# Performance work log

Hardware: AMD Instinct MI355X
Metric: run time of the kernel (lower is better)

Reference implementation:

```python
import jax, jax.numpy as jnp
import numpy as np

B = 100000      # query points
L = 8           # num levels
N_RBF = 256     # RBF centers per level
F = 16          # features per level
OUT = 3         # output dim


def setup_inputs() -> dict:
    key = jax.random.key(0)
    k = jax.random.split(key, 6)
    x = jax.random.normal(k[0], (B, 3), dtype=jnp.float32)
    # small-magnitude features so gaussian RBF responses are non-degenerate
    feats = 0.1 * jax.random.normal(k[1], (B, L * F), dtype=jnp.float32)
    # centers initialized uniform(-1e-4, 1e-4) as in the torch module
    centers = jax.random.uniform(k[2], (L, N_RBF, F), dtype=jnp.float32,
                                 minval=-1e-4, maxval=1e-4)
    # log-width parameters (exp'd in forward); small perturbation around 0
    betas = 0.01 * jax.random.normal(k[3], (L, N_RBF, F), dtype=jnp.float32)
    W = jax.random.normal(k[4], (OUT, N_RBF * L), dtype=jnp.float32) / np.sqrt(N_RBF * L)
    b = jax.random.normal(k[5], (OUT,), dtype=jnp.float32) * 0.01
    return {"x": x, "feats": feats, "centers": centers, "betas": betas, "W": W, "b": b}


def reference(x, feats, centers, betas, W, b):
    # centers, betas: [L, N, F]. x is unused by the original forward (faithful).
    Lnum, N, f = centers.shape
    rbfs = []
    for i in range(Lnum):
        # concat of first i+1 per-level tables along feature axis -> [N, (i+1)*f]
        C = centers[: i + 1].transpose(1, 0, 2).reshape(N, (i + 1) * f)
        Bw = jnp.exp(betas[: i + 1].transpose(1, 0, 2).reshape(N, (i + 1) * f))
        x_in = feats[:, : (i + 1) * f]                      # [B, (i+1)*f]
        term1 = (x_in * x_in) @ Bw.T                        # [B, N]
        term2 = x_in @ (Bw * C).T                           # [B, N]
        term3 = jnp.sum(Bw * C * C, axis=1)                 # [N]
        dist_sq = term1 - 2.0 * term2 + term3[None, :]
        rbfs.append(jnp.exp(-0.5 * dist_sq))                # gaussian basis
    outs = jnp.concatenate(rbfs, axis=-1)                   # [B, L*N]
    return outs @ W.T + b
```

## Files before the change

kernel.cpp:

```cpp
#include <hip/hip_runtime.h>
#include <math.h>

#define LN 8
#define NRBF 256
#define FD 16
#define OUTD 3

typedef __attribute__((ext_vector_type(8))) short short8;
typedef __attribute__((ext_vector_type(4))) float floatx4;

__device__ __forceinline__ short f2bf(float f) {
    unsigned u = __builtin_bit_cast(unsigned, f);
    u += 0x7fffu + ((u >> 16) & 1u);
    return (short)(u >> 16);
}


__global__ __launch_bounds__(256) void prep(
    const float* __restrict__ centers, const float* __restrict__ betas,
    const float* __restrict__ W, short* __restrict__ PKB, float* __restrict__ EPI)
{
    int t = blockIdx.x * 256 + threadIdx.x;
    if (t < 8192) {
        int lane = t & 63;
        int nt   = (t >> 6) & 15;
        int j    = t >> 10;
        int n    = nt * 16 + (lane & 15);
        int kq   = lane >> 4;
        short8 v;
#pragma unroll
        for (int e = 0; e < 8; ++e) {
            int k = kq * 8 + e;
            int m = k >> 1;
            int p = k & 1;
            size_t idx = ((size_t)(j * NRBF + n)) * FD + m;
            float a = __expf(betas[idx]);
            float c = centers[idx];
            v[e] = f2bf(p ? (-2.0f * a * c) : a);
        }
        *((short8*)(PKB + (size_t)t * 8)) = v;
    }
    if (t < 2048) {
        int j = t >> 8;
        int n = t & 255;
        float t3 = 0.f;
        for (int jj = 0; jj <= j; ++jj)
#pragma unroll
            for (int m = 0; m < FD; ++m) {
                size_t idx = ((size_t)(jj * NRBF + n)) * FD + m;
                float a = __expf(betas[idx]);
                float c = centers[idx];
                t3 = fmaf(a * c, c, t3);
            }
        int nt = n >> 4, l = n & 15;
        float* e = EPI + ((size_t)((j * 16 + nt) * 16 + l)) * 4;
        e[0] = -0.72134752f * t3;
        e[1] = W[0 * (LN * NRBF) + j * NRBF + n];
        e[2] = W[1 * (LN * NRBF) + j * NRBF + n];
        e[3] = W[2 * (LN * NRBF) + j * NRBF + n];
    }
}

__global__ __launch_bounds__(256, 2) void rbf_mfma(
    const float* __restrict__ feats, const short* __restrict__ PKB,
    const float* __restrict__ EPI, const float* __restrict__ bias,
    float* __restrict__ out, int B)
{
    int lane = threadIdx.x & 63;
    int wid  = threadIdx.x >> 6;
    int ntile_total = (B + 15) >> 4;
    int tile = blockIdx.x * 4 + wid;
    if (tile >= ntile_total) return;
    int b0 = tile * 16;
    int m  = lane & 15;
    int kq = lane >> 4;

    int brow = b0 + m; if (brow >= B) brow = B - 1;
    const float* xrow = feats + (size_t)brow * (LN * FD) + kq * 4;
    short8 afrag[LN];
#pragma unroll
    for (int j = 0; j < LN; ++j) {
        float4 x = *((const float4*)(xrow + j * FD));
        short8 f;
        f[0] = f2bf(x.x * x.x); f[1] = f2bf(x.x);
        f[2] = f2bf(x.y * x.y); f[3] = f2bf(x.y);
        f[4] = f2bf(x.z * x.z); f[5] = f2bf(x.z);
        f[6] = f2bf(x.w * x.w); f[7] = f2bf(x.w);
        afrag[j] = f;
    }

    const short8* pb = (const short8*)PKB;
    const float4* ep = (const float4*)EPI;
    const float KC = -0.72134752f;

    float oacc[12];
#pragma unroll
    for (int i = 0; i < 12; ++i) oacc[i] = 0.f;

#pragma unroll 1
    for (int nt = 0; nt < 16; ++nt) {
        floatx4 acc = {0.f, 0.f, 0.f, 0.f};
#pragma unroll
        for (int j = 0; j < LN; ++j) {
            short8 bfrag = pb[(size_t)(j * 16 + nt) * 64 + lane];
            acc = __builtin_amdgcn_mfma_f32_16x16x32_bf16(afrag[j], bfrag, acc, 0, 0, 0);
            float4 e = ep[(size_t)(j * 16 + nt) * 16 + m];
#pragma unroll
            for (int r = 0; r < 4; ++r) {
                float rv = __builtin_amdgcn_exp2f(fmaf(acc[r], KC, e.x));
                oacc[r * 3 + 0] = fmaf(rv, e.y, oacc[r * 3 + 0]);
                oacc[r * 3 + 1] = fmaf(rv, e.z, oacc[r * 3 + 1]);
                oacc[r * 3 + 2] = fmaf(rv, e.w, oacc[r * 3 + 2]);
            }
        }
    }

#pragma unroll
    for (int i = 0; i < 12; ++i) {
        oacc[i] += __shfl_xor(oacc[i], 1);
        oacc[i] += __shfl_xor(oacc[i], 2);
        oacc[i] += __shfl_xor(oacc[i], 4);
        oacc[i] += __shfl_xor(oacc[i], 8);
    }

    if (m < OUTD) {
        float bv = bias[m];
#pragma unroll
        for (int r = 0; r < 4; ++r) {
            int row = b0 + kq * 4 + r;
            float v = (m == 0) ? oacc[r * 3 + 0] : (m == 1) ? oacc[r * 3 + 1] : oacc[r * 3 + 2];
            if (row < B) out[(size_t)row * OUTD + m] = v + bv;
        }
    }
}

extern "C" void kernel_launch(void* const* d_in, const int* in_sizes, int n_in,
                              void* d_out, int out_size, void* d_ws, size_t ws_size,
                              hipStream_t stream) {
    const float* feats   = (const float*)d_in[1];
    const float* centers = (const float*)d_in[2];
    const float* betas   = (const float*)d_in[3];
    const float* W       = (const float*)d_in[4];
    const float* bias    = (const float*)d_in[5];
    float* out = (float*)d_out;
    int B = in_sizes[1] / (LN * FD);

    short* PKB = (short*)d_ws;
    float* EPI = (float*)((char*)d_ws + 65536 * 2);

    prep<<<32, 256, 0, stream>>>(centers, betas, W, PKB, EPI);

    int tiles  = (B + 15) / 16;
    int blocks = (tiles + 3) / 4;
    rbf_mfma<<<blocks, 256, 0, stream>>>(feats, PKB, EPI, bias, out, B);
}
```

Baseline: 171.4 us.

## Split prep kernels, stage epilogue in LDS, double-buffer B fragments in RBF kernel

```diff
diff --git a/kernel.cpp b/kernel.cpp
--- a/kernel.cpp
+++ b/kernel.cpp
@@ -16,61 +16,85 @@
 }
 
 
-__global__ __launch_bounds__(256) void prep(
+#define KC (-0.72134752044f)
+
+__global__ __launch_bounds__(256) void prep_pkb(
     const float* __restrict__ centers, const float* __restrict__ betas,
-    const float* __restrict__ W, short* __restrict__ PKB, float* __restrict__ EPI)
+    short* __restrict__ PKB)
 {
     int t = blockIdx.x * 256 + threadIdx.x;
-    if (t < 8192) {
-        int lane = t & 63;
-        int nt   = (t >> 6) & 15;
-        int j    = t >> 10;
-        int n    = nt * 16 + (lane & 15);
-        int kq   = lane >> 4;
-        short8 v;
+    int lane = t & 63;
+    int nt   = (t >> 6) & 15;
+    int j    = t >> 10;
+    int n    = nt * 16 + (lane & 15);
+    int kq   = lane >> 4;
+    size_t base = ((size_t)(j * NRBF + n)) * FD + kq * 4;
+    float4 bq = *(const float4*)(betas + base);
+    float4 cq = *(const float4*)(centers + base);
+    float a0 = __expf(bq.x), a1 = __expf(bq.y), a2 = __expf(bq.z), a3 = __expf(bq.w);
+    short8 v;
+    v[0] = f2bf(a0); v[1] = f2bf(-2.0f * a0 * cq.x);
+    v[2] = f2bf(a1); v[3] = f2bf(-2.0f * a1 * cq.y);
+    v[4] = f2bf(a2); v[5] = f2bf(-2.0f * a2 * cq.z);
+    v[6] = f2bf(a3); v[7] = f2bf(-2.0f * a3 * cq.w);
+    *((short8*)(PKB + (size_t)t * 8)) = v;
+}
+
+__global__ __launch_bounds__(1024) void prep_epi(
+    const float* __restrict__ centers, const float* __restrict__ betas,
+    const float* __restrict__ W, float* __restrict__ EPI)
+{
+    __shared__ float ls[LN * NRBF];
+    int t = threadIdx.x;
 #pragma unroll
-        for (int e = 0; e < 8; ++e) {
-            int k = kq * 8 + e;
-            int m = k >> 1;
-            int p = k & 1;
-            size_t idx = ((size_t)(j * NRBF + n)) * FD + m;
-            float a = __expf(betas[idx]);
-            float c = centers[idx];
-            v[e] = f2bf(p ? (-2.0f * a * c) : a);
+    for (int h = 0; h < 2; ++h) {
+        int p = t + h * 1024;
+        const float* bp = betas   + (size_t)p * FD;
+        const float* cp = centers + (size_t)p * FD;
+        float s = 0.f;
+#pragma unroll
+        for (int q = 0; q < 4; ++q) {
+            float4 bq = *(const float4*)(bp + q * 4);
+            float4 cq = *(const float4*)(cp + q * 4);
+            s = fmaf(__expf(bq.x) * cq.x, cq.x, s);
+            s = fmaf(__expf(bq.y) * cq.y, cq.y, s);
+            s = fmaf(__expf(bq.z) * cq.z, cq.z, s);
+            s = fmaf(__expf(bq.w) * cq.w, cq.w, s);
         }
-        *((short8*)(PKB + (size_t)t * 8)) = v;
+        ls[p] = s;
     }
-    if (t < 2048) {
-        int j = t >> 8;
-        int n = t & 255;
+    __syncthreads();
+#pragma unroll
+    for (int h = 0; h < 2; ++h) {
+        int p = t + h * 1024;
+        int j = p >> 8, n = p & 255;
         float t3 = 0.f;
-        for (int jj = 0; jj <= j; ++jj)
-#pragma unroll
-            for (int m = 0; m < FD; ++m) {
-                size_t idx = ((size_t)(jj * NRBF + n)) * FD + m;
-                float a = __expf(betas[idx]);
-                float c = centers[idx];
-                t3 = fmaf(a * c, c, t3);
-            }
+        for (int jj = 0; jj <= j; ++jj) t3 += ls[jj * 256 + n];
         int nt = n >> 4, l = n & 15;
-        float* e = EPI + ((size_t)((j * 16 + nt) * 16 + l)) * 4;
-        e[0] = -0.72134752f * t3;
-        e[1] = W[0 * (LN * NRBF) + j * NRBF + n];
-        e[2] = W[1 * (LN * NRBF) + j * NRBF + n];
-        e[3] = W[2 * (LN * NRBF) + j * NRBF + n];
+        float4 e;
+        e.x = KC * t3;
+        e.y = W[0 * (LN * NRBF) + j * NRBF + n];
+        e.z = W[1 * (LN * NRBF) + j * NRBF + n];
+        e.w = W[2 * (LN * NRBF) + j * NRBF + n];
+        ((float4*)EPI)[(j * 16 + nt) * 16 + l] = e;
     }
 }
 
-__global__ __launch_bounds__(256, 2) void rbf_mfma(
+__global__ __launch_bounds__(256, 3) void rbf_mfma(
     const float* __restrict__ feats, const short* __restrict__ PKB,
     const float* __restrict__ EPI, const float* __restrict__ bias,
     float* __restrict__ out, int B)
 {
+    __shared__ float4 eps_s[LN * 16 * 16];
+    for (int i = threadIdx.x; i < LN * 16 * 16; i += 256)
+        eps_s[i] = ((const float4*)EPI)[i];
+
     int lane = threadIdx.x & 63;
     int wid  = threadIdx.x >> 6;
     int ntile_total = (B + 15) >> 4;
     int tile = blockIdx.x * 4 + wid;
-    if (tile >= ntile_total) return;
+    bool tvalid = (tile < ntile_total);
+    if (!tvalid) tile = ntile_total - 1;
     int b0 = tile * 16;
     int m  = lane & 15;
     int kq = lane >> 4;
@@ -89,22 +113,30 @@
         afrag[j] = f;
     }
 
-    const short8* pb = (const short8*)PKB;
-    const float4* ep = (const float4*)EPI;
-    const float KC = -0.72134752f;
+    const short8* pb = (const short8*)PKB + lane;
+
+    short8 buf[2][LN];
+#pragma unroll
+    for (int j = 0; j < LN; ++j) buf[0][j] = pb[(j * 16 + 0) * 64];
 
     float oacc[12];
 #pragma unroll
     for (int i = 0; i < 12; ++i) oacc[i] = 0.f;
 
-#pragma unroll 1
+    __syncthreads();
+
+#pragma unroll 2
     for (int nt = 0; nt < 16; ++nt) {
+        int cur = nt & 1, nx = cur ^ 1;
+        if (nt < 15) {
+#pragma unroll
+            for (int j = 0; j < LN; ++j) buf[nx][j] = pb[(j * 16 + nt + 1) * 64];
+        }
         floatx4 acc = {0.f, 0.f, 0.f, 0.f};
 #pragma unroll
         for (int j = 0; j < LN; ++j) {
-            short8 bfrag = pb[(size_t)(j * 16 + nt) * 64 + lane];
-            acc = __builtin_amdgcn_mfma_f32_16x16x32_bf16(afrag[j], bfrag, acc, 0, 0, 0);
-            float4 e = ep[(size_t)(j * 16 + nt) * 16 + m];
+            acc = __builtin_amdgcn_mfma_f32_16x16x32_bf16(afrag[j], buf[cur][j], acc, 0, 0, 0);
+            float4 e = eps_s[(j * 16 + nt) * 16 + m];
 #pragma unroll
             for (int r = 0; r < 4; ++r) {
                 float rv = __builtin_amdgcn_exp2f(fmaf(acc[r], KC, e.x));
@@ -123,7 +155,7 @@
         oacc[i] += __shfl_xor(oacc[i], 8);
     }
 
-    if (m < OUTD) {
+    if (tvalid && m < OUTD) {
         float bv = bias[m];
 #pragma unroll
         for (int r = 0; r < 4; ++r) {
@@ -148,7 +180,8 @@
     short* PKB = (short*)d_ws;
     float* EPI = (float*)((char*)d_ws + 65536 * 2);
 
-    prep<<<32, 256, 0, stream>>>(centers, betas, W, PKB, EPI);
+    prep_pkb<<<32, 256, 0, stream>>>(centers, betas, PKB);
+    prep_epi<<<1, 1024, 0, stream>>>(centers, betas, W, EPI);
 
     int tiles  = (B + 15) / 16;
     int blocks = (tiles + 3) / 4;
```

Result: slower. 231.4 us (+35.0%).
